# Kernel tuning notes

Hardware: AMD Instinct MI355X
Metric: run time of the kernel (lower is better)

Reference implementation:

```python
import jax, jax.numpy as jnp
import numpy as np

B, C, L = 8, 512, 2048


def setup_inputs() -> dict:
    key = jax.random.key(0)
    ks = jax.random.split(key, 7)
    s = 1.0 / np.sqrt(C)
    return {
        "x": jax.random.normal(ks[0], (B, C, L), dtype=jnp.float32),
        "Wq": jax.random.normal(ks[1], (C, C), dtype=jnp.float32) * s,
        "bq": jax.random.normal(ks[2], (C,), dtype=jnp.float32) * s,
        "Wk": jax.random.normal(ks[3], (C, C), dtype=jnp.float32) * s,
        "bk": jax.random.normal(ks[4], (C,), dtype=jnp.float32) * s,
        "Wv": jax.random.normal(ks[5], (C, C), dtype=jnp.float32) * s,
        "bv": jax.random.normal(ks[6], (C,), dtype=jnp.float32) * s,
    }


def reference(x, Wq, bq, Wk, bk, Wv, bv):
    # Conv1d(kernel_size=1) == per-position linear: [C_out, C_in] @ x[b,:,l]
    q = jnp.einsum('oi,bil->bol', Wq, x) + bq[None, :, None]  # [B, C, L]
    k = jnp.einsum('oi,bil->bol', Wk, x) + bk[None, :, None]
    v = jnp.einsum('oi,bil->bol', Wv, x) + bv[None, :, None]
    scale = 1.0 / jnp.sqrt(jnp.asarray(x.shape[1], dtype=x.dtype))
    # scores[b, l, m] = sum_c q[b,c,l] * k[b,c,m] / sqrt(C)
    scores = jnp.einsum('bcl,bcm->blm', q, k) * scale  # [B, L, L]
    attn = jax.nn.softmax(scores, axis=-1)
    # out[b, c, l] = sum_m v[b,c,m] * attn[b,l,m]   (== bmm(V, attn^T))
    return jnp.einsum('bcm,blm->bcl', v, attn)  # [B, C, L]
```

## Files before the change

### kernel.cpp

```cpp
#include <hip/hip_runtime.h>
#include <hip/hip_bf16.h>
#include <math.h>

#define B 8
#define C 512
#define L 2048

using bf16x8 = __bf16 __attribute__((ext_vector_type(8)));
using f32x4  = float __attribute__((ext_vector_type(4)));

#define MFMA(a, b, c) __builtin_amdgcn_mfma_f32_16x16x32_bf16((a), (b), (c), 0, 0, 0)
#define SCALE 0.044194173824159216f

__device__ __forceinline__ unsigned short f2bf(float f) {
    __hip_bfloat16 h = __float2bfloat16(f);
    return *reinterpret_cast<unsigned short*>(&h);
}
__device__ __forceinline__ void load_lds16(const unsigned short* g, unsigned short* l) {
    __builtin_amdgcn_global_load_lds(
        (const __attribute__((address_space(1))) unsigned int*)g,
        (__attribute__((address_space(3))) unsigned int*)l, 16, 0, 0);
}

template<int MODE, int KDIM>
__device__ __forceinline__ void gemm_core(
    const unsigned short* __restrict__ A,
    const unsigned short* __restrict__ Bm,
    unsigned short* As, unsigned short* Bs,
    void* __restrict__ OutV, int ldo,
    float* __restrict__ ep)
{
    const int t = threadIdx.x;
    const int wave = t >> 6, lane = t & 63;
    const int ll = t & 15, quad = (t >> 4) & 3;
    const int lr = lane >> 2, chunk = lane & 3;
    const int wm = (wave & 1) * 64, wn = (wave >> 1) * 64;

    const unsigned short* gA0 = A  + (size_t)(wave * 32 + lr) * KDIM + chunk * 8;
    const unsigned short* gB0 = Bm + (size_t)(wave * 32 + lr) * KDIM + chunk * 8;
    unsigned short* lA0 = As + (wave * 32) * 32;
    unsigned short* lB0 = Bs + (wave * 32) * 32;

    f32x4 acc[4][4];
#pragma unroll
    for (int i = 0; i < 4; ++i)
#pragma unroll
        for (int j = 0; j < 4; ++j) acc[i][j] = (f32x4){0.f, 0.f, 0.f, 0.f};

#pragma unroll 1
    for (int k0 = 0; k0 < KDIM; k0 += 32) {
        __syncthreads();
        load_lds16(gA0 + k0, lA0);
        load_lds16(gA0 + (size_t)16 * KDIM + k0, lA0 + 16 * 32);
        load_lds16(gB0 + k0, lB0);
        load_lds16(gB0 + (size_t)16 * KDIM + k0, lB0 + 16 * 32);
        __syncthreads();

        bf16x8 af[4], bf[4];
#pragma unroll
        for (int mi = 0; mi < 4; ++mi)
            af[mi] = *(const bf16x8*)&As[(wm + mi * 16 + ll) * 32 + quad * 8];
#pragma unroll
        for (int ni = 0; ni < 4; ++ni)
            bf[ni] = *(const bf16x8*)&Bs[(wn + ni * 16 + ll) * 32 + quad * 8];
#pragma unroll
        for (int mi = 0; mi < 4; ++mi)
#pragma unroll
            for (int ni = 0; ni < 4; ++ni)
                acc[mi][ni] = MFMA(af[mi], bf[ni], acc[mi][ni]);
    }

    float rpart[4][4];
    if (MODE == 2) {
#pragma unroll
        for (int mi = 0; mi < 4; ++mi)
#pragma unroll
            for (int r = 0; r < 4; ++r) rpart[mi][r] = 0.f;
    }

#pragma unroll
    for (int mi = 0; mi < 4; ++mi)
#pragma unroll
        for (int ni = 0; ni < 4; ++ni) {
            const int col = wn + ni * 16 + ll;
            float epc = 0.f;
            if (MODE == 0) epc = ep[col];
            if (MODE == 3) epc = 1.0f / ep[col];
#pragma unroll
            for (int r = 0; r < 4; ++r) {
                const int row = wm + mi * 16 + quad * 4 + r;
                float v = acc[mi][ni][r];
                if (MODE == 0)      v += epc;
                else if (MODE == 1) v += ep[row];
                else if (MODE == 2) { v = __expf(v * SCALE - 12.f); rpart[mi][r] += v; }
                else                v *= epc;
                if (MODE == 3)
                    ((float*)OutV)[(size_t)row * ldo + col] = v;
                else
                    ((unsigned short*)OutV)[(size_t)row * ldo + col] = f2bf(v);
            }
        }

    if (MODE == 2) {
#pragma unroll
        for (int mi = 0; mi < 4; ++mi)
#pragma unroll
            for (int r = 0; r < 4; ++r) {
                float s = rpart[mi][r];
                s += __shfl_xor(s, 1, 64);
                s += __shfl_xor(s, 2, 64);
                s += __shfl_xor(s, 4, 64);
                s += __shfl_xor(s, 8, 64);
                if (ll == 0) atomicAdd(ep + wm + mi * 16 + quad * 4 + r, s);
            }
    }
}

__global__ __launch_bounds__(256) void xpose_cvt(
    const float* __restrict__ x, unsigned short* __restrict__ xt)
{
    __shared__ float tile[64][69];
    const int b = blockIdx.z, l0 = blockIdx.x * 64, c0 = blockIdx.y * 64;
    const int t = threadIdx.x;
    const int lx = t & 15, cy = t >> 4;
    const float* xb = x + (size_t)b * C * L;
#pragma unroll
    for (int p = 0; p < 4; ++p) {
        float4 v = *(const float4*)(xb + (size_t)(c0 + p * 16 + cy) * L + l0 + lx * 4);
        tile[p * 16 + cy][lx * 4 + 0] = v.x;
        tile[p * 16 + cy][lx * 4 + 1] = v.y;
        tile[p * 16 + cy][lx * 4 + 2] = v.z;
        tile[p * 16 + cy][lx * 4 + 3] = v.w;
    }
    __syncthreads();
    const int ocl = t & 15, ot = t >> 4;
    unsigned short* xtb = xt + (size_t)b * L * C;
#pragma unroll
    for (int p = 0; p < 4; ++p) {
        int ol = p * 16 + ot;
        union { unsigned short h[4]; uint2 u; } pk;
#pragma unroll
        for (int i = 0; i < 4; ++i) pk.h[i] = f2bf(tile[ocl * 4 + i][ol]);
        *(uint2*)(xtb + (size_t)(l0 + ol) * C + c0 + ocl * 4) = pk.u;
    }
}

__global__ __launch_bounds__(256) void wcvt(
    const float* __restrict__ Wq, const float* __restrict__ Wk,
    const float* __restrict__ Wv, unsigned short* __restrict__ o)
{
    const int i = (blockIdx.x * 256 + threadIdx.x) * 4;
    const int which = i >> 18;
    const int off = i & 0x3FFFF;
    const float* src = (which == 0) ? Wq : (which == 1) ? Wk : Wv;
    float4 v = *(const float4*)(src + off);
    union { unsigned short h[4]; uint2 u; } pk;
    pk.h[0] = f2bf(v.x); pk.h[1] = f2bf(v.y); pk.h[2] = f2bf(v.z); pk.h[3] = f2bf(v.w);
    *(uint2*)(o + i) = pk.u;
}

__global__ __launch_bounds__(256) void qkv_gemm(
    const unsigned short* __restrict__ xt, const unsigned short* __restrict__ Wb,
    const float* __restrict__ bq, const float* __restrict__ bk,
    const float* __restrict__ bv,
    unsigned short* __restrict__ Qt, unsigned short* __restrict__ Kt,
    unsigned short* __restrict__ Vv)
{
    __shared__ unsigned short As[128 * 32], Bs[128 * 32];
    const int id = blockIdx.x;
    const int b = id & 7, r = id >> 3;
    const int which = r >> 6, tt = r & 63;
    const unsigned short* xtb = xt + (size_t)b * L * C;
    if (which < 2) {
        const int m0 = (tt & 15) * 128, n0 = (tt >> 4) * 128;
        const unsigned short* A  = xtb + (size_t)m0 * C;
        const unsigned short* Bm = Wb + (size_t)which * C * C + (size_t)n0 * C;
        unsigned short* Out = (which ? Kt : Qt) + (size_t)b * L * C
                              + (size_t)m0 * C + n0;
        gemm_core<0, C>(A, Bm, As, Bs, Out, C,
                        const_cast<float*>((which ? bk : bq) + n0));
    } else {
        const int m0 = (tt & 3) * 128, n0 = (tt >> 2) * 128;
        const unsigned short* A  = Wb + (size_t)2 * C * C + (size_t)m0 * C;
        const unsigned short* Bm = xtb + (size_t)n0 * C;
        unsigned short* Out = Vv + (size_t)b * C * L + (size_t)m0 * L + n0;
        gemm_core<1, C>(A, Bm, As, Bs, Out, L, const_cast<float*>(bv + m0));
    }
}

__global__ __launch_bounds__(256) void sc_exp(
    const unsigned short* __restrict__ Qt, const unsigned short* __restrict__ Kt,
    unsigned short* __restrict__ P, float* __restrict__ rsum,
    int hoff, int qrows, int mshift)
{
    __shared__ unsigned short As[128 * 32], Bs[128 * 32];
    const int id = blockIdx.x;
    const int b = id & 7, r = id >> 3;
    const int m0 = (r & ((1 << mshift) - 1)) * 128, n0 = (r >> mshift) * 128;
    const unsigned short* A  = Qt + (size_t)b * L * C + (size_t)(hoff + m0) * C;
    const unsigned short* Bm = Kt + (size_t)b * L * C + (size_t)n0 * C;
    unsigned short* Out = P + (size_t)b * qrows * L + (size_t)m0 * L + n0;
    float* ep = rsum + (size_t)b * L + hoff + m0;
    gemm_core<2, C>(A, Bm, As, Bs, Out, L, ep);
}

__global__ __launch_bounds__(256) void pv_gemm(
    const unsigned short* __restrict__ Vv, const unsigned short* __restrict__ P,
    const float* __restrict__ rsum, float* __restrict__ out,
    int hoff, int qrows)
{
    __shared__ unsigned short As[128 * 32], Bs[128 * 32];
    const int id = blockIdx.x;
    const int b = id & 7, r = id >> 3;
    const int m0 = (r & 3) * 128, n0 = (r >> 2) * 128;
    const unsigned short* A  = Vv + (size_t)b * C * L + (size_t)m0 * L;
    const unsigned short* Bm = P + (size_t)b * qrows * L + (size_t)n0 * L;
    float* Out = out + (size_t)b * C * L + (size_t)m0 * L + hoff + n0;
    float* ep = const_cast<float*>(rsum) + (size_t)b * L + hoff + n0;
    gemm_core<3, L>(A, Bm, As, Bs, Out, L, ep);
}

extern "C" void kernel_launch(void* const* d_in, const int* in_sizes, int n_in,
                              void* d_out, int out_size, void* d_ws, size_t ws_size,
                              hipStream_t stream) {
    const float* x  = (const float*)d_in[0];
    const float* Wq = (const float*)d_in[1];
    const float* bq = (const float*)d_in[2];
    const float* Wk = (const float*)d_in[3];
    const float* bk = (const float*)d_in[4];
    const float* Wv = (const float*)d_in[5];
    const float* bv = (const float*)d_in[6];
    float* out = (float*)d_out;

    const size_t BCL = (size_t)B * C * L;
    const bool fullP = ws_size >= 119078912ull;

    unsigned short* Qt = (unsigned short*)d_ws;
    unsigned short* Kt = Qt + BCL;
    unsigned short* Vv = Kt + BCL;
    unsigned short *Wb, *xt, *P;
    float* rsum;
    if (fullP) {
        Wb   = Vv + BCL;
        rsum = (float*)(Wb + (size_t)3 * C * C);
        xt   = (unsigned short*)(rsum + (size_t)B * L);
        P    = xt;
    } else {
        xt   = Vv + BCL;
        P    = xt;
        Wb   = P + (size_t)B * 1024 * L;
        rsum = (float*)(Wb + (size_t)3 * C * C);
    }

    hipMemsetAsync(rsum, 0, (size_t)B * L * 4, stream);
    xpose_cvt<<<dim3(L / 64, C / 64, B), 256, 0, stream>>>(x, xt);
    wcvt<<<dim3(3 * C * C / 1024), 256, 0, stream>>>(Wq, Wk, Wv, Wb);
    qkv_gemm<<<dim3(1536), 256, 0, stream>>>(xt, Wb, bq, bk, bv, Qt, Kt, Vv);

    if (fullP) {
        sc_exp<<<dim3(2048), 256, 0, stream>>>(Qt, Kt, P, rsum, 0, L, 4);
        pv_gemm<<<dim3(512), 256, 0, stream>>>(Vv, P, rsum, out, 0, L);
    } else {
        for (int h = 0; h < 2; ++h) {
            sc_exp<<<dim3(1024), 256, 0, stream>>>(Qt, Kt, P, rsum, h * 1024, 1024, 3);
            pv_gemm<<<dim3(256), 256, 0, stream>>>(Vv, P, rsum, out, h * 1024, 1024);
        }
    }
}
```

Measured before the change: 246.8 us.

## Double K-step per barrier, fold rsum zeroing into wcvt, use exp2 and manual bf16 rounding

The GEMM core now loads 64 K-elements per barrier pair, as two 32-wide LDS planes, which halves the number of __syncthreads and widens each global-to-LDS batch. The LDS arrays double in size, which may lower occupancy. The rsum memset is folded into the wcvt kernel to save a launch. The softmax exponent becomes a single fma plus exp2f with prescaled constants, and bf16 conversion is replaced with inline round-to-nearest-even bit arithmetic.

```diff
diff --git a/kernel.cpp b/kernel.cpp
--- a/kernel.cpp
+++ b/kernel.cpp
@@ -10,11 +10,13 @@
 using f32x4  = float __attribute__((ext_vector_type(4)));
 
 #define MFMA(a, b, c) __builtin_amdgcn_mfma_f32_16x16x32_bf16((a), (b), (c), 0, 0, 0)
-#define SCALE 0.044194173824159216f
+#define SC2 0.06375872f
+#define SH2 -17.312340f
 
 __device__ __forceinline__ unsigned short f2bf(float f) {
-    __hip_bfloat16 h = __float2bfloat16(f);
-    return *reinterpret_cast<unsigned short*>(&h);
+    unsigned int u; __builtin_memcpy(&u, &f, 4);
+    u += 0x7FFF + ((u >> 16) & 1);
+    return (unsigned short)(u >> 16);
 }
 __device__ __forceinline__ void load_lds16(const unsigned short* g, unsigned short* l) {
     __builtin_amdgcn_global_load_lds(
@@ -40,6 +42,7 @@
     const unsigned short* gB0 = Bm + (size_t)(wave * 32 + lr) * KDIM + chunk * 8;
     unsigned short* lA0 = As + (wave * 32) * 32;
     unsigned short* lB0 = Bs + (wave * 32) * 32;
+    const int P1 = 128 * 32;
 
     f32x4 acc[4][4];
 #pragma unroll
@@ -48,26 +51,33 @@
         for (int j = 0; j < 4; ++j) acc[i][j] = (f32x4){0.f, 0.f, 0.f, 0.f};
 
 #pragma unroll 1
-    for (int k0 = 0; k0 < KDIM; k0 += 32) {
+    for (int k0 = 0; k0 < KDIM; k0 += 64) {
         __syncthreads();
         load_lds16(gA0 + k0, lA0);
         load_lds16(gA0 + (size_t)16 * KDIM + k0, lA0 + 16 * 32);
+        load_lds16(gA0 + k0 + 32, lA0 + P1);
+        load_lds16(gA0 + (size_t)16 * KDIM + k0 + 32, lA0 + P1 + 16 * 32);
         load_lds16(gB0 + k0, lB0);
         load_lds16(gB0 + (size_t)16 * KDIM + k0, lB0 + 16 * 32);
+        load_lds16(gB0 + k0 + 32, lB0 + P1);
+        load_lds16(gB0 + (size_t)16 * KDIM + k0 + 32, lB0 + P1 + 16 * 32);
         __syncthreads();
 
-        bf16x8 af[4], bf[4];
-#pragma unroll
-        for (int mi = 0; mi < 4; ++mi)
-            af[mi] = *(const bf16x8*)&As[(wm + mi * 16 + ll) * 32 + quad * 8];
-#pragma unroll
-        for (int ni = 0; ni < 4; ++ni)
-            bf[ni] = *(const bf16x8*)&Bs[(wn + ni * 16 + ll) * 32 + quad * 8];
-#pragma unroll
-        for (int mi = 0; mi < 4; ++mi)
+#pragma unroll
+        for (int p = 0; p < 2; ++p) {
+            bf16x8 af[4], bf[4];
+#pragma unroll
+            for (int mi = 0; mi < 4; ++mi)
+                af[mi] = *(const bf16x8*)&As[p * P1 + (wm + mi * 16 + ll) * 32 + quad * 8];
 #pragma unroll
             for (int ni = 0; ni < 4; ++ni)
-                acc[mi][ni] = MFMA(af[mi], bf[ni], acc[mi][ni]);
+                bf[ni] = *(const bf16x8*)&Bs[p * P1 + (wn + ni * 16 + ll) * 32 + quad * 8];
+#pragma unroll
+            for (int mi = 0; mi < 4; ++mi)
+#pragma unroll
+                for (int ni = 0; ni < 4; ++ni)
+                    acc[mi][ni] = MFMA(af[mi], bf[ni], acc[mi][ni]);
+        }
     }
 
     float rpart[4][4];
@@ -92,7 +102,7 @@
                 float v = acc[mi][ni][r];
                 if (MODE == 0)      v += epc;
                 else if (MODE == 1) v += ep[row];
-                else if (MODE == 2) { v = __expf(v * SCALE - 12.f); rpart[mi][r] += v; }
+                else if (MODE == 2) { v = exp2f(fmaf(v, SC2, SH2)); rpart[mi][r] += v; }
                 else                v *= epc;
                 if (MODE == 3)
                     ((float*)OutV)[(size_t)row * ldo + col] = v;
@@ -147,8 +157,13 @@
 
 __global__ __launch_bounds__(256) void wcvt(
     const float* __restrict__ Wq, const float* __restrict__ Wk,
-    const float* __restrict__ Wv, unsigned short* __restrict__ o)
-{
+    const float* __restrict__ Wv, unsigned short* __restrict__ o,
+    float* __restrict__ rsum)
+{
+    if (blockIdx.x < 16) {
+        float4 z = make_float4(0.f, 0.f, 0.f, 0.f);
+        *(float4*)(rsum + (blockIdx.x * 256 + threadIdx.x) * 4) = z;
+    }
     const int i = (blockIdx.x * 256 + threadIdx.x) * 4;
     const int which = i >> 18;
     const int off = i & 0x3FFFF;
@@ -166,7 +181,7 @@
     unsigned short* __restrict__ Qt, unsigned short* __restrict__ Kt,
     unsigned short* __restrict__ Vv)
 {
-    __shared__ unsigned short As[128 * 32], Bs[128 * 32];
+    __shared__ unsigned short As[2 * 128 * 32], Bs[2 * 128 * 32];
     const int id = blockIdx.x;
     const int b = id & 7, r = id >> 3;
     const int which = r >> 6, tt = r & 63;
@@ -193,7 +208,7 @@
     unsigned short* __restrict__ P, float* __restrict__ rsum,
     int hoff, int qrows, int mshift)
 {
-    __shared__ unsigned short As[128 * 32], Bs[128 * 32];
+    __shared__ unsigned short As[2 * 128 * 32], Bs[2 * 128 * 32];
     const int id = blockIdx.x;
     const int b = id & 7, r = id >> 3;
     const int m0 = (r & ((1 << mshift) - 1)) * 128, n0 = (r >> mshift) * 128;
@@ -209,7 +224,7 @@
     const float* __restrict__ rsum, float* __restrict__ out,
     int hoff, int qrows)
 {
-    __shared__ unsigned short As[128 * 32], Bs[128 * 32];
+    __shared__ unsigned short As[2 * 128 * 32], Bs[2 * 128 * 32];
     const int id = blockIdx.x;
     const int b = id & 7, r = id >> 3;
     const int m0 = (r & 3) * 128, n0 = (r >> 2) * 128;
@@ -252,9 +267,8 @@
         rsum = (float*)(Wb + (size_t)3 * C * C);
     }
 
-    hipMemsetAsync(rsum, 0, (size_t)B * L * 4, stream);
     xpose_cvt<<<dim3(L / 64, C / 64, B), 256, 0, stream>>>(x, xt);
-    wcvt<<<dim3(3 * C * C / 1024), 256, 0, stream>>>(Wq, Wk, Wv, Wb);
+    wcvt<<<dim3(3 * C * C / 1024), 256, 0, stream>>>(Wq, Wk, Wv, Wb, rsum);
     qkv_gemm<<<dim3(1536), 256, 0, stream>>>(xt, Wb, bq, bk, bv, Qt, Kt, Vv);
 
     if (fullP) {
```

Result: faster. 231.3 us (-6.3%).
